# Performance work log

Hardware: AMD Instinct MI355X
Metric: run time of the kernel (lower is better)

Reference implementation:

```python
import jax, jax.numpy as jnp
import numpy as np

NUM_FEATURE = 512
HIDDEN = 256
NUM_CLASSES = 10
L1 = 1e-4
ALPHA = 1e-3
BATCH = 65536


def setup_inputs() -> dict:
    key = jax.random.key(0)
    k = jax.random.split(key, 6)
    x = jax.random.normal(k[0], (BATCH, NUM_FEATURE), dtype=jnp.float32)
    y = jax.random.randint(k[1], (BATCH,), 0, NUM_CLASSES, dtype=jnp.int32)
    fc0 = jax.random.normal(k[2], (NUM_FEATURE, 512), dtype=jnp.float32) / NUM_FEATURE
    fc1 = jax.random.normal(k[3], (NUM_FEATURE, 512), dtype=jnp.float32) / NUM_FEATURE
    w = jax.random.normal(k[4], (NUM_FEATURE, HIDDEN), dtype=jnp.float32) / NUM_FEATURE
    w1 = jax.random.normal(k[5], (HIDDEN, NUM_CLASSES), dtype=jnp.float32) / HIDDEN
    return {"x": x, "y": y, "fc0": fc0, "fc1": fc1, "w": w, "w1": w1}


def reference(x, y, fc0, fc1, w, w1):
    # sigmoid-gated MLP block with residual
    x1 = x @ fc0                                   # [B, 512]
    x2 = jax.nn.relu(x @ fc1)                      # [B, 512]
    x4 = x + (1.0 + jax.nn.sigmoid(x1)) * x2       # [B, 512] residual

    # head (Dropout(p=0.0) is identity)
    logits = jax.nn.relu(x4 @ w) @ w1              # [B, 10]
    pred = jnp.argmax(logits, axis=1)

    # cross-entropy (mean over batch)
    logp = jax.nn.log_softmax(logits, axis=-1)
    ce = -jnp.mean(jnp.take_along_axis(logp, y[:, None].astype(jnp.int32), axis=1))

    # L1 penalty on all weight matrices
    l1_pen = L1 * (jnp.abs(w1).sum() + jnp.abs(w).sum()
                   + jnp.abs(fc0).sum() + jnp.abs(fc1).sum())

    # per-class variance: sum_i ||mean_{y_i} - x4_i||^2, vectorized via segment sums
    counts = jax.ops.segment_sum(jnp.ones((x4.shape[0],), jnp.float32), y,
                                 num_segments=NUM_CLASSES)
    sums = jax.ops.segment_sum(x4, y, num_segments=NUM_CLASSES)   # [10, 512]
    means = sums / jnp.maximum(counts, 1.0)[:, None]
    var_loss = jnp.sum(jnp.square(means[y] - x4))

    loss = ce + l1_pen + ALPHA * var_loss
    acc = jnp.mean((pred.astype(jnp.int32) == y.astype(jnp.int32)).astype(jnp.float32))
    return (loss, acc)
```

## Files before the change

### kernel.cpp

```cpp
#include <hip/hip_runtime.h>
#include <stdint.h>

#define BATCH 65536
#define FDIM 512
#define HDIM 256
#define NC 10
#define NREP 16

typedef short short8 __attribute__((ext_vector_type(8)));
typedef float f32x4 __attribute__((ext_vector_type(4)));

#define OFF_FC0T   ((size_t)0)
#define OFF_FC1T   (OFF_FC0T + (size_t)512*512*2)
#define OFF_WT     (OFF_FC1T + (size_t)512*512*2)
#define OFF_XT     (OFF_WT   + (size_t)256*512*2)
#define OFF_X4T    (OFF_XT   + (size_t)BATCH*512*2)
#define OFF_ACC    (OFF_X4T  + (size_t)BATCH*512*2)
#define SCAL_SUMSQ 0
#define SCAL_CE    16
#define SCAL_ACC   32
#define SCAL_L1    48
#define SCAL_CTR   64
#define SCAL_N     128
#define CNT_OFF    SCAL_N
#define GSUM_OFF   (SCAL_N + NREP*16)
#define ACC_FLOATS (GSUM_OFF + NREP*5120)
#define OFF_W1T    (OFF_ACC + (size_t)ACC_FLOATS*4)

#define GLL(g,l) __builtin_amdgcn_global_load_lds((const __attribute__((address_space(1))) void*)(g), (__attribute__((address_space(3))) void*)(l), 16, 0, 0)

__device__ __forceinline__ unsigned short f2b(float f){
  unsigned u = __float_as_uint(f);
  u += 0x7FFFu + ((u >> 16) & 1u);
  return (unsigned short)(u >> 16);
}
__device__ __forceinline__ float b2f(unsigned short h){
  return __uint_as_float(((unsigned)h) << 16);
}
__device__ __forceinline__ unsigned pk2b(float f0, float f1){
  unsigned u0 = __float_as_uint(f0) + 0x8000u;
  unsigned u1 = __float_as_uint(f1) + 0x8000u;
  return __builtin_amdgcn_perm(u1, u0, 0x07060302u);
}
__device__ __forceinline__ float ald(const float* p){
  return __hip_atomic_load(p, __ATOMIC_RELAXED, __HIP_MEMORY_SCOPE_AGENT);
}

__global__ __launch_bounds__(256) void k_setup(
    const float* __restrict__ x,   const float* __restrict__ fc0,
    const float* __restrict__ fc1, const float* __restrict__ w,
    const float* __restrict__ w1,  const int* __restrict__ y,
    unsigned short* __restrict__ xT,   unsigned short* __restrict__ fc0T,
    unsigned short* __restrict__ fc1T, unsigned short* __restrict__ wT,
    unsigned short* __restrict__ w1T,  float* __restrict__ accb)
{
  int blk = blockIdx.x, t = threadIdx.x;
  if (blk < 2048){
    __shared__ __align__(16) unsigned short xls[16*520];
    int wv = t >> 6, l = t & 63;
    #pragma unroll 1
    for (int it = 0; it < 2; ++it){
      int I = blk*2 + it;
      #pragma unroll
      for (int rr = 0; rr < 4; ++rr){
        int row = wv*4 + rr;
        const float* src = x + ((size_t)(I*16 + row))*FDIM + l*8;
        float4 v0 = *(const float4*)src;
        float4 v1 = *(const float4*)(src + 4);
        unsigned o[4];
        o[0] = pk2b(v0.x, v0.y); o[1] = pk2b(v0.z, v0.w);
        o[2] = pk2b(v1.x, v1.y); o[3] = pk2b(v1.z, v1.w);
        *(short8*)&xls[row*520 + l*8] = *(short8*)o;
      }
      __syncthreads();
      #pragma unroll
      for (int cc = 0; cc < 4; ++cc){
        int C = cc*4 + wv;
        short8 v = *(const short8*)&xls[(l & 15)*520 + C*32 + (l >> 4)*8];
        *(short8*)&xT[(((size_t)I*16 + C) << 9) + l*8] = v;
      }
      __syncthreads();
    }
    return;
  }
  if (blk < 2384){
    int i = (blk - 2048)*256 + t;
    float l1v = 0.f;
    if (i < 32768){
      int n4 = i&15, m = (i>>4)&3, C = (i>>6)&15, J = i>>10;
      int n = J*16+n4, k8 = C*4+m;
      unsigned short o[8];
      #pragma unroll
      for (int j=0;j<8;++j){ float v = fc0[(size_t)(k8*8+j)*512 + n]; o[j]=f2b(v); l1v += fabsf(v); }
      *(short8*)&fc0T[(size_t)(J*16+C)*512 + (i&63)*8] = *(short8*)o;
    } else if (i < 65536){
      int j0 = i - 32768;
      int n4 = j0&15, m = (j0>>4)&3, C = (j0>>6)&15, J = j0>>10;
      int n = J*16+n4, k8 = C*4+m;
      unsigned short o[8];
      #pragma unroll
      for (int j=0;j<8;++j){ float v = fc1[(size_t)(k8*8+j)*512 + n]; o[j]=f2b(v); l1v += fabsf(v); }
      *(short8*)&fc1T[(size_t)(J*16+C)*512 + (j0&63)*8] = *(short8*)o;
    } else if (i < 81920){
      int j0 = i - 65536;
      int n4 = j0&15, m = (j0>>4)&3, C = (j0>>6)&15, J = j0>>10;
      int n = J*16+n4, k8 = C*4+m;
      unsigned short o[8];
      #pragma unroll
      for (int j=0;j<8;++j){ float v = w[(size_t)(k8*8+j)*256 + n]; o[j]=f2b(v); l1v += fabsf(v); }
      *(short8*)&wT[(size_t)(J*16+C)*512 + (j0&63)*8] = *(short8*)o;
    } else if (i < 86016){
      int j0 = i - 81920;
      int C = j0 >> 9, l = (j0 >> 3) & 63, e = j0 & 7;
      int n = l & 15, k = C*32 + (l>>4)*8 + e;
      float v = (n < NC) ? w1[k*NC + n] : 0.f;
      w1T[C*512 + l*8 + e] = f2b(v);
      if (n < NC) l1v = fabsf(v);
    }
    for (int off = 32; off; off >>= 1) l1v += __shfl_down(l1v, off);
    if ((t & 63) == 0 && l1v != 0.f)
      atomicAdd(&accb[SCAL_L1 + (blk & (NREP-1))], l1v);
    return;
  }
  if (blk < 2465){
    int base = (blk - 2384)*1024;
    #pragma unroll
    for (int j=0;j<4;++j){
      int idx = base + j*256 + t;
      if (idx < ACC_FLOATS && (idx < CNT_OFF || idx >= CNT_OFF + NREP*16))
        accb[idx] = 0.f;
    }
    return;
  }
  {
    __shared__ float cntS[16];
    int b = blk - 2465;
    if (t < 16) cntS[t] = 0.f;
    __syncthreads();
    int base = b*4096;
    for (int i = t; i < 4096; i += 256) atomicAdd(&cntS[y[base+i]], 1.f);
    __syncthreads();
    if (t < 16) accb[CNT_OFF + b*16 + t] = cntS[t];
  }
}

__global__ __launch_bounds__(512, 4) void k_gemm12(
    const unsigned short* __restrict__ xT,
    const unsigned short* __restrict__ fc0T,
    const unsigned short* __restrict__ fc1T,
    const int* __restrict__ y,
    unsigned short* __restrict__ x4T,
    float* __restrict__ accb)
{
  extern __shared__ __align__(16) char ldsd[];
  float* scal = accb;
  float* gsum = accb + GSUM_OFF;

  int blk = blockIdx.x;
  int wg = (blk & 7)*256 + (blk >> 3);
  int rowblk = wg >> 2;
  int colblk = wg & 3;

  int t = threadIdx.x;
  int wv = t >> 6, lane = t & 63, ln = lane & 15, quad = lane >> 4;
  int wr = wv >> 2, wc = wv & 3;

  const char* xb  = (const char*)xT;
  const char* b0b = (const char*)fc0T;
  const char* b1b = (const char*)fc1T;

  const f32x4 zv = {0.f,0.f,0.f,0.f};
  f32x4 acc1[4][2], acc2[4][2];
  #pragma unroll
  for (int m=0;m<4;++m){ acc1[m][0]=zv; acc1[m][1]=zv; acc2[m][0]=zv; acc2[m][1]=zv; }

  short8 a[4], b0r[2], b1r[2];

  GLL(xb  + (((size_t)((rowblk*8+wv)*16 + 0)) << 10) + lane*16, ldsd +         (wv<<10) + lane*16);
  GLL(b0b + (((size_t)((colblk*8+wv)*16 + 0)) << 10) + lane*16, ldsd +  8192 + (wv<<10) + lane*16);
  GLL(b1b + (((size_t)((colblk*8+wv)*16 + 0)) << 10) + lane*16, ldsd + 16384 + (wv<<10) + lane*16);
  asm volatile("s_waitcnt vmcnt(0)" ::: "memory");
  __builtin_amdgcn_sched_barrier(0);
  __builtin_amdgcn_s_barrier();

  #pragma unroll
  for (int kt = 0; kt < 16; ++kt){
    char* cur = ldsd + ((kt & 1) ? 24576 : 0);
    char* nxt = ldsd + ((kt & 1) ? 0 : 24576);
    if (kt < 15){
      GLL(xb  + (((size_t)((rowblk*8+wv)*16 + kt+1)) << 10) + lane*16, nxt +         (wv<<10) + lane*16);
      GLL(b0b + (((size_t)((colblk*8+wv)*16 + kt+1)) << 10) + lane*16, nxt +  8192 + (wv<<10) + lane*16);
      GLL(b1b + (((size_t)((colblk*8+wv)*16 + kt+1)) << 10) + lane*16, nxt + 16384 + (wv<<10) + lane*16);
    }
    #pragma unroll
    for (int m=0;m<4;++m)
      a[m] = *(const short8*)(cur + ((wr*4+m)<<10) + lane*16);
    #pragma unroll
    for (int n=0;n<2;++n){
      b0r[n] = *(const short8*)(cur +  8192 + ((wc*2+n)<<10) + lane*16);
      b1r[n] = *(const short8*)(cur + 16384 + ((wc*2+n)<<10) + lane*16);
    }
    asm volatile("s_waitcnt lgkmcnt(0)" ::: "memory");
    __builtin_amdgcn_sched_barrier(0);
    __builtin_amdgcn_s_setprio(1);
    #pragma unroll
    for (int n=0;n<2;++n)
      #pragma unroll
      for (int m=0;m<4;++m){
        acc1[m][n] = __builtin_amdgcn_mfma_f32_16x16x32_bf16(a[m], b0r[n], acc1[m][n], 0,0,0);
        acc2[m][n] = __builtin_amdgcn_mfma_f32_16x16x32_bf16(a[m], b1r[n], acc2[m][n], 0,0,0);
      }
    __builtin_amdgcn_s_setprio(0);
    if (kt < 15){ asm volatile("s_waitcnt vmcnt(0)" ::: "memory"); }
    __builtin_amdgcn_sched_barrier(0);
    __builtin_amdgcn_s_barrier();
  }

  #pragma unroll
  for (int c = 0; c < 4; ++c){
    GLL(xb + (((size_t)((rowblk*8+wv)*16 + colblk*4 + c)) << 10) + lane*16,
        ldsd + ((wv*4 + c) << 10) + lane*16);
  }
  asm volatile("s_waitcnt vmcnt(0)" ::: "memory");
  __syncthreads();

  unsigned short* resU = (unsigned short*)ldsd;
  unsigned short* x4U  = (unsigned short*)(ldsd + 32768);
  float sumsq = 0.f;
  #pragma unroll
  for (int m = 0; m < 4; ++m){
    #pragma unroll
    for (int n = 0; n < 2; ++n){
      #pragma unroll
      for (int r = 0; r < 4; ++r){
        int slot = (quad*4 + r) | ((n*2 + (ln>>3)) << 4);
        int idx = (((wr*4 + m)*4 + wc) << 9) + slot*8 + (ln & 7);
        float xv  = b2f(resU[idx]);
        float x1v = acc1[m][n][r];
        float x2v = fmaxf(acc2[m][n][r], 0.f);
        float gate = 1.f + 1.f/(1.f + __expf(-x1v));
        float x4v = fmaf(gate, x2v, xv);
        unsigned short ub = f2b(x4v);
        float fq = b2f(ub);
        sumsq = fmaf(fq, fq, sumsq);
        x4U[idx] = ub;
        acc1[m][n][r] = fq;
      }
    }
  }
  for (int off = 32; off; off >>= 1) sumsq += __shfl_down(sumsq, off);
  __syncthreads();

  float cs[NC][2];
  #pragma unroll
  for (int c=0;c<NC;++c){ cs[c][0]=0.f; cs[c][1]=0.f; }
  {
    const int* yrow = y + rowblk*128 + wr*64;
    #pragma unroll
    for (int m = 0; m < 4; ++m){
      int yv[4];
      #pragma unroll
      for (int r = 0; r < 4; ++r) yv[r] = yrow[m*16 + quad*4 + r];
      #pragma unroll
      for (int r = 0; r < 4; ++r){
        float v0 = acc1[m][0][r], v1 = acc1[m][1][r];
        #pragma unroll
        for (int c = 0; c < NC; ++c){
          bool msk = (yv[r] == c);
          cs[c][0] += msk ? v0 : 0.f;
          cs[c][1] += msk ? v1 : 0.f;
        }
      }
    }
  }
  #pragma unroll
  for (int c = 0; c < NC; ++c)
    #pragma unroll
    for (int n = 0; n < 2; ++n){
      cs[c][n] += __shfl_xor(cs[c][n], 16);
      cs[c][n] += __shfl_xor(cs[c][n], 32);
    }
  if (lane < 16){
    size_t gb = (size_t)(blk & (NREP-1))*5120 + colblk*128 + wc*32 + ln;
    #pragma unroll
    for (int c = 0; c < NC; ++c){
      atomicAdd(&gsum[gb + c*512],      cs[c][0]);
      atomicAdd(&gsum[gb + c*512 + 16], cs[c][1]);
    }
  }

  float* red = (float*)ldsd;
  if (lane == 0) red[wv] = sumsq;
  __syncthreads();
  if (t == 0){
    float s = 0.f;
    #pragma unroll
    for (int i=0;i<8;++i) s += red[i];
    atomicAdd(&scal[SCAL_SUMSQ + (blk & (NREP-1))], s);
  }
  #pragma unroll
  for (int r = 0; r < 4; ++r){
    int o = r*512 + t;
    int tile = o >> 6, off16 = o & 63;
    int Il = tile >> 2, Cl = tile & 3;
    size_t Ig = (size_t)rowblk*8 + Il;
    int Cg = colblk*4 + Cl;
    *(short8*)&x4T[((Ig*16 + Cg) << 9) + off16*8] =
      *(const short8*)&x4U[(tile << 9) + off16*8];
  }
}


#define BARRIER() __builtin_amdgcn_s_barrier()
#define LGKM0() do{ asm volatile("s_waitcnt lgkmcnt(0)" ::: "memory"); \
                    __builtin_amdgcn_sched_barrier(0); }while(0)

#define RA(AB, C) do{                                                         \
  _Pragma("unroll") for (int m_=0;m_<8;++m_)                                  \
    a[m_] = *(const short8*)((AB) + (((wr*8+m_)*2 + (C))<<10) + lane*16);     \
}while(0)

#define RB(AB, MAT, C) do{                                                    \
  _Pragma("unroll") for (int n_=0;n_<2;++n_)                                  \
    bb[n_] = *(const short8*)((AB) + 32768 + (MAT)*16384 +                    \
                              (((wc*2+n_)*2 + (C))<<10) + lane*16);           \
}while(0)

#define MM16(ACC) do{                                                         \
  __builtin_amdgcn_s_setprio(1);                                              \
  _Pragma("unroll") for (int n_=0;n_<2;++n_)                                  \
  _Pragma("unroll") for (int m_=0;m_<8;++m_)                                  \
    ACC[m_][n_] = __builtin_amdgcn_mfma_f32_16x16x32_bf16(a[m_], bb[n_], ACC[m_][n_], 0,0,0); \
  __builtin_amdgcn_s_setprio(0);                                              \
}while(0)

#define SA(KT, C) do{                                                         \
  char* d_ = ldsd + (((KT)&1) ? 65536 : 0);                                   \
  _Pragma("unroll") for (int r_=0;r_<2;++r_){                                 \
    int I_ = wv + r_*8;                                                       \
    GLL(xb + (((size_t)((rowblk*16 + I_)*16 + (KT)*2 + (C))) << 10) + lane*16,\
        d_ + ((I_*2 + (C)) << 10) + lane*16);                                 \
  } }while(0)

#define SB(KT, C) do{                                                         \
  char* d_ = ldsd + (((KT)&1) ? 65536 : 0) + 32768;                           \
  GLL(b0b + (((size_t)((colblk*8 + wv)*16 + (KT)*2 + (C))) << 10) + lane*16,  \
      d_ + ((wv*2 + (C)) << 10) + lane*16);                                   \
  GLL(b1b + (((size_t)((colblk*8 + wv)*16 + (KT)*2 + (C))) << 10) + lane*16,  \
      d_ + 16384 + ((wv*2 + (C)) << 10) + lane*16);                           \
}while(0)

#define KLOOP() do{                                                           \
  SA(0,0); SB(0,0); SA(0,1); SB(0,1); SA(1,0); SB(1,0); SA(1,1);              \
  asm volatile("s_waitcnt vmcnt(6)" ::: "memory");                            \
  __builtin_amdgcn_sched_barrier(0);                                          \
  BARRIER();                                                                  \
  _Pragma("unroll")                                                           \
  for (int i = 0; i < 4; ++i){                                                \
    int kt0 = 2*i, kt1 = 2*i+1;                                               \
    char* Ab0 = ldsd + ((kt0 & 1) ? 65536 : 0);                               \
    char* Ab1 = ldsd + ((kt1 & 1) ? 65536 : 0);                               \
    RA(Ab0, 0); RB(Ab0, 0, 0);                                                \
    SB(kt1, 1);                                                               \
    BARRIER(); LGKM0(); MM16(acc1);                                           \
    BARRIER();                                                                \
    RB(Ab0, 1, 0);                                                            \
    if (i < 3) SA(kt0+2, 0);                                                  \
    BARRIER(); LGKM0(); MM16(acc2);                                           \
    BARRIER();                                                                \
    RA(Ab0, 1); RB(Ab0, 0, 1);                                                \
    if (i < 3) SB(kt0+2, 0);                                                  \
    BARRIER(); LGKM0(); MM16(acc1);                                           \
    BARRIER();                                                                \
    RB(Ab0, 1, 1);                                                            \
    if (i < 3) SA(kt0+2, 1);                                                  \
    BARRIER(); LGKM0(); MM16(acc2);                                           \
    if (i < 3) { asm volatile("s_waitcnt vmcnt(6)" ::: "memory"); }           \
    else       { asm volatile("s_waitcnt vmcnt(0)" ::: "memory"); }           \
    __builtin_amdgcn_sched_barrier(0);                                        \
    BARRIER();                                                                \
    RA(Ab1, 0); RB(Ab1, 0, 0);                                                \
    if (i < 3) SB(kt0+2, 1);                                                  \
    BARRIER(); LGKM0(); MM16(acc1);                                           \
    BARRIER();                                                                \
    RB(Ab1, 1, 0);                                                            \
    if (i < 3) SA(kt1+2, 0);                                                  \
    BARRIER(); LGKM0(); MM16(acc2);                                           \
    BARRIER();                                                                \
    RA(Ab1, 1); RB(Ab1, 0, 1);                                                \
    if (i < 3) SB(kt1+2, 0);                                                  \
    BARRIER(); LGKM0(); MM16(acc1);                                           \
    BARRIER();                                                                \
    RB(Ab1, 1, 1);                                                            \
    if (i < 3) SA(kt1+2, 1);                                                  \
    BARRIER(); LGKM0(); MM16(acc2);                                           \
    if (i < 3) { asm volatile("s_waitcnt vmcnt(6)" ::: "memory");             \
                 __builtin_amdgcn_sched_barrier(0); }                         \
    BARRIER();                                                                \
  }                                                                           \
}while(0)

__global__ __launch_bounds__(512, 2) void k_gemm3_head(
    const unsigned short* __restrict__ x4T,
    const unsigned short* __restrict__ wT,
    const unsigned short* __restrict__ w1T,
    const int* __restrict__ y,
    float* __restrict__ accb,
    float* __restrict__ out)
{
  extern __shared__ __align__(16) char ldsd[];
  __shared__ float redc[8], reda[8];
  __shared__ int lastB;

  float* scal = accb;

  int blk = blockIdx.x;
  int rowblk = blk;
  const int colblk = 0;

  int t = threadIdx.x;
  int wv = t >> 6, lane = t & 63, ln = lane & 15, quad = lane >> 4;
  int wr = wv >> 2, wc = wv & 3;
  int rep = (blk ^ (blk >> 4)) & (NREP-1);

  const char* xb  = (const char*)x4T;
  const char* b0b = (const char*)wT;
  const char* b1b = (const char*)wT + (size_t)128*1024;

  const f32x4 zv = {0.f,0.f,0.f,0.f};
  f32x4 acc1[8][2], acc2[8][2];
  #pragma unroll
  for (int m=0;m<8;++m){ acc1[m][0]=zv; acc1[m][1]=zv; acc2[m][0]=zv; acc2[m][1]=zv; }

  short8 a[8], bb[2];

  KLOOP();

  short8 bw1[8];
  #pragma unroll
  for (int Ck = 0; Ck < 8; ++Ck)
    bw1[Ck] = *(const short8*)&w1T[Ck*512 + lane*8];

  unsigned short* transH = (unsigned short*)ldsd;
  #pragma unroll
  for (int m = 0; m < 8; ++m){
    #pragma unroll
    for (int n = 0; n < 2; ++n){
      #pragma unroll
      for (int r = 0; r < 4; ++r){
        int slot = (quad*4 + r) | ((n*2 + (ln>>3)) << 4);
        int e = ln & 7;
        int IhA = wr*8 + m;
        transH[((IhA*8 + wc)     << 9) + slot*8 + e] = f2b(fmaxf(acc1[m][n][r], 0.f));
        transH[((IhA*8 + 4 + wc) << 9) + slot*8 + e] = f2b(fmaxf(acc2[m][n][r], 0.f));
      }
    }
  }
  __syncthreads();

  f32x4 alog[2] = {zv, zv};
  #pragma unroll
  for (int ih = 0; ih < 2; ++ih){
    int Ih = wv*2 + ih;
    #pragma unroll
    for (int Ck = 0; Ck < 8; ++Ck){
      short8 af = *(const short8*)&transH[((Ih*8 + Ck) << 9) + lane*8];
      alog[ih] = __builtin_amdgcn_mfma_f32_16x16x32_bf16(af, bw1[Ck], alog[ih], 0,0,0);
    }
  }

  float ce_l = 0.f, acc_l = 0.f;
  #pragma unroll
  for (int ih = 0; ih < 2; ++ih){
    #pragma unroll
    for (int r = 0; r < 4; ++r){
      int grow = blk*256 + (wv*2 + ih)*16 + quad*4 + r;
      int yv = y[grow];
      float lg = (ln < NC) ? alog[ih][r] : -1e30f;
      float m = lg; int mi = ln;
      #pragma unroll
      for (int mk = 1; mk < 16; mk <<= 1){
        float om = __shfl_xor(m, mk); int oi = __shfl_xor(mi, mk);
        if (om > m || (om == m && oi < mi)){ m = om; mi = oi; }
      }
      float e  = (ln < NC) ? __expf(lg - m) : 0.f;
      float sy = (ln == yv) ? lg : 0.f;
      #pragma unroll
      for (int mk = 1; mk < 16; mk <<= 1){ e += __shfl_xor(e, mk); sy += __shfl_xor(sy, mk); }
      float lse = m + __logf(e);
      if (ln == 0){ ce_l += (lse - sy); acc_l += (mi == yv) ? 1.f : 0.f; }
    }
  }
  ce_l  += __shfl_down(ce_l, 16);  acc_l += __shfl_down(acc_l, 16);
  ce_l  += __shfl_down(ce_l, 32);  acc_l += __shfl_down(acc_l, 32);
  if (lane == 0){ redc[wv] = ce_l; reda[wv] = acc_l; }
  __syncthreads();
  if (t == 0){
    float c = 0.f, aa = 0.f;
    #pragma unroll
    for (int i=0;i<8;++i){ c += redc[i]; aa += reda[i]; }
    atomicAdd(&scal[SCAL_CE  + rep], c);
    atomicAdd(&scal[SCAL_ACC + rep], aa);
    __threadfence();
    int prev = atomicAdd((int*)(scal + SCAL_CTR), 1);
    lastB = (prev == (int)gridDim.x - 1);
  }
  __syncthreads();
  if (!lastB) return;

  {
    const float* gsum = accb + GSUM_OFF;
    const float* gcnt = accb + CNT_OFF;
    float contrib = 0.f;
    for (int idx = t; idx < 5120; idx += 512){
      float S = 0.f;
      #pragma unroll
      for (int r = 0; r < NREP; ++r) S += ald(&gsum[(size_t)r*5120 + idx]);
      int c = idx >> 9;
      float cnt = 0.f;
      #pragma unroll
      for (int r = 0; r < NREP; ++r) cnt += ald(&gcnt[r*16 + c]);
      contrib += S*S / fmaxf(cnt, 1.f);
    }
    for (int off = 32; off; off >>= 1) contrib += __shfl_down(contrib, off);
    __syncthreads();
    if (lane == 0) redc[wv] = contrib;
    __syncthreads();
    if (t == 0){
      float var2 = 0.f;
      #pragma unroll
      for (int i=0;i<8;++i) var2 += redc[i];
      float sumsq=0.f, ce=0.f, accv=0.f, l1=0.f;
      for (int r=0;r<NREP;++r){
        sumsq += ald(&scal[SCAL_SUMSQ+r]);
        ce    += ald(&scal[SCAL_CE+r]);
        accv  += ald(&scal[SCAL_ACC+r]);
        l1    += ald(&scal[SCAL_L1+r]);
      }
      float var_loss = sumsq - var2;
      out[0] = ce/(float)BATCH + 1e-4f*l1 + 1e-3f*var_loss;
      out[1] = accv/(float)BATCH;
    }
  }
}

extern "C" void kernel_launch(void* const* d_in, const int* in_sizes, int n_in,
                              void* d_out, int out_size, void* d_ws, size_t ws_size,
                              hipStream_t stream){
  (void)in_sizes; (void)n_in; (void)out_size; (void)ws_size;
  const float* x   = (const float*)d_in[0];
  const int*   y   = (const int*)d_in[1];
  const float* fc0 = (const float*)d_in[2];
  const float* fc1 = (const float*)d_in[3];
  const float* w   = (const float*)d_in[4];
  const float* w1  = (const float*)d_in[5];
  char* ws = (char*)d_ws;
  unsigned short* fc0T = (unsigned short*)(ws + OFF_FC0T);
  unsigned short* fc1T = (unsigned short*)(ws + OFF_FC1T);
  unsigned short* wT   = (unsigned short*)(ws + OFF_WT);
  unsigned short* xT   = (unsigned short*)(ws + OFF_XT);
  unsigned short* x4T  = (unsigned short*)(ws + OFF_X4T);
  unsigned short* w1T  = (unsigned short*)(ws + OFF_W1T);
  float* accb = (float*)(ws + OFF_ACC);

  static bool once = [](){
    hipFuncSetAttribute((const void*)k_gemm12,
                        hipFuncAttributeMaxDynamicSharedMemorySize, 65536);
    hipFuncSetAttribute((const void*)k_gemm3_head,
                        hipFuncAttributeMaxDynamicSharedMemorySize, 131072);
    return true;
  }();
  (void)once;

  k_setup<<<2481, 256, 0, stream>>>(x, fc0, fc1, w, w1, y, xT, fc0T, fc1T, wT, w1T, accb);
  k_gemm12<<<2048, 512, 65536, stream>>>(xT, fc0T, fc1T, y, x4T, accb);
  k_gemm3_head<<<256, 512, 131072, stream>>>(x4T, wT, w1T, y, accb, (float*)d_out);
}
```

Baseline: 352.2 us.

## Fuse x fp32-to-bf16 conversion into gemm12 A-tile loads, drop xT pre-pass

Removes the separate setup pass that converted x to a bf16 tiled copy (xT) and instead has k_gemm12 read fp32 x directly into registers, pack it to bf16 and write it into LDS each k-step. This drops one full write and read of a 64 MB bf16 copy of x plus the setup blocks for it. In exchange, each of the 4 column blocks re-reads the fp32 row tile (twice the bytes of bf16), the A loads are now register-staged rather than direct-to-LDS, and the residual reload also reads fp32.

```diff
diff --git a/kernel.cpp b/kernel.cpp
--- a/kernel.cpp
+++ b/kernel.cpp
@@ -13,8 +13,7 @@
 #define OFF_FC0T   ((size_t)0)
 #define OFF_FC1T   (OFF_FC0T + (size_t)512*512*2)
 #define OFF_WT     (OFF_FC1T + (size_t)512*512*2)
-#define OFF_XT     (OFF_WT   + (size_t)256*512*2)
-#define OFF_X4T    (OFF_XT   + (size_t)BATCH*512*2)
+#define OFF_X4T    (OFF_WT   + (size_t)256*512*2)
 #define OFF_ACC    (OFF_X4T  + (size_t)BATCH*512*2)
 #define SCAL_SUMSQ 0
 #define SCAL_CE    16
@@ -47,44 +46,16 @@
 }
 
 __global__ __launch_bounds__(256) void k_setup(
-    const float* __restrict__ x,   const float* __restrict__ fc0,
-    const float* __restrict__ fc1, const float* __restrict__ w,
-    const float* __restrict__ w1,  const int* __restrict__ y,
-    unsigned short* __restrict__ xT,   unsigned short* __restrict__ fc0T,
-    unsigned short* __restrict__ fc1T, unsigned short* __restrict__ wT,
-    unsigned short* __restrict__ w1T,  float* __restrict__ accb)
+    const float* __restrict__ fc0, const float* __restrict__ fc1,
+    const float* __restrict__ w,   const float* __restrict__ w1,
+    const int* __restrict__ y,
+    unsigned short* __restrict__ fc0T, unsigned short* __restrict__ fc1T,
+    unsigned short* __restrict__ wT,   unsigned short* __restrict__ w1T,
+    float* __restrict__ accb)
 {
   int blk = blockIdx.x, t = threadIdx.x;
-  if (blk < 2048){
-    __shared__ __align__(16) unsigned short xls[16*520];
-    int wv = t >> 6, l = t & 63;
-    #pragma unroll 1
-    for (int it = 0; it < 2; ++it){
-      int I = blk*2 + it;
-      #pragma unroll
-      for (int rr = 0; rr < 4; ++rr){
-        int row = wv*4 + rr;
-        const float* src = x + ((size_t)(I*16 + row))*FDIM + l*8;
-        float4 v0 = *(const float4*)src;
-        float4 v1 = *(const float4*)(src + 4);
-        unsigned o[4];
-        o[0] = pk2b(v0.x, v0.y); o[1] = pk2b(v0.z, v0.w);
-        o[2] = pk2b(v1.x, v1.y); o[3] = pk2b(v1.z, v1.w);
-        *(short8*)&xls[row*520 + l*8] = *(short8*)o;
-      }
-      __syncthreads();
-      #pragma unroll
-      for (int cc = 0; cc < 4; ++cc){
-        int C = cc*4 + wv;
-        short8 v = *(const short8*)&xls[(l & 15)*520 + C*32 + (l >> 4)*8];
-        *(short8*)&xT[(((size_t)I*16 + C) << 9) + l*8] = v;
-      }
-      __syncthreads();
-    }
-    return;
-  }
-  if (blk < 2384){
-    int i = (blk - 2048)*256 + t;
+  if (blk < 336){
+    int i = blk*256 + t;
     float l1v = 0.f;
     if (i < 32768){
       int n4 = i&15, m = (i>>4)&3, C = (i>>6)&15, J = i>>10;
@@ -122,8 +93,8 @@
       atomicAdd(&accb[SCAL_L1 + (blk & (NREP-1))], l1v);
     return;
   }
-  if (blk < 2465){
-    int base = (blk - 2384)*1024;
+  if (blk < 417){
+    int base = (blk - 336)*1024;
     #pragma unroll
     for (int j=0;j<4;++j){
       int idx = base + j*256 + t;
@@ -134,7 +105,7 @@
   }
   {
     __shared__ float cntS[16];
-    int b = blk - 2465;
+    int b = blk - 417;
     if (t < 16) cntS[t] = 0.f;
     __syncthreads();
     int base = b*4096;
@@ -145,7 +116,7 @@
 }
 
 __global__ __launch_bounds__(512, 4) void k_gemm12(
-    const unsigned short* __restrict__ xT,
+    const float* __restrict__ x,
     const unsigned short* __restrict__ fc0T,
     const unsigned short* __restrict__ fc1T,
     const int* __restrict__ y,
@@ -165,9 +136,9 @@
   int wv = t >> 6, lane = t & 63, ln = lane & 15, quad = lane >> 4;
   int wr = wv >> 2, wc = wv & 3;
 
-  const char* xb  = (const char*)xT;
   const char* b0b = (const char*)fc0T;
   const char* b1b = (const char*)fc1T;
+  const float* arow = x + (size_t)(rowblk*128 + wv*16 + ln)*FDIM + quad*8;
 
   const f32x4 zv = {0.f,0.f,0.f,0.f};
   f32x4 acc1[4][2], acc2[4][2];
@@ -176,19 +147,28 @@
 
   short8 a[4], b0r[2], b1r[2];
 
-  GLL(xb  + (((size_t)((rowblk*8+wv)*16 + 0)) << 10) + lane*16, ldsd +         (wv<<10) + lane*16);
-  GLL(b0b + (((size_t)((colblk*8+wv)*16 + 0)) << 10) + lane*16, ldsd +  8192 + (wv<<10) + lane*16);
-  GLL(b1b + (((size_t)((colblk*8+wv)*16 + 0)) << 10) + lane*16, ldsd + 16384 + (wv<<10) + lane*16);
-  asm volatile("s_waitcnt vmcnt(0)" ::: "memory");
-  __builtin_amdgcn_sched_barrier(0);
-  __builtin_amdgcn_s_barrier();
+  {
+    float4 va0 = *(const float4*)(arow);
+    float4 va1 = *(const float4*)(arow + 4);
+    GLL(b0b + (((size_t)((colblk*8+wv)*16 + 0)) << 10) + lane*16, ldsd +  8192 + (wv<<10) + lane*16);
+    GLL(b1b + (((size_t)((colblk*8+wv)*16 + 0)) << 10) + lane*16, ldsd + 16384 + (wv<<10) + lane*16);
+    unsigned o[4];
+    o[0] = pk2b(va0.x, va0.y); o[1] = pk2b(va0.z, va0.w);
+    o[2] = pk2b(va1.x, va1.y); o[3] = pk2b(va1.z, va1.w);
+    *(short8*)(ldsd + (wv<<10) + lane*16) = *(short8*)o;
+    asm volatile("s_waitcnt vmcnt(0) lgkmcnt(0)" ::: "memory");
+    __builtin_amdgcn_sched_barrier(0);
+    __builtin_amdgcn_s_barrier();
+  }
 
   #pragma unroll
   for (int kt = 0; kt < 16; ++kt){
     char* cur = ldsd + ((kt & 1) ? 24576 : 0);
     char* nxt = ldsd + ((kt & 1) ? 0 : 24576);
+    float4 va0, va1;
     if (kt < 15){
-      GLL(xb  + (((size_t)((rowblk*8+wv)*16 + kt+1)) << 10) + lane*16, nxt +         (wv<<10) + lane*16);
+      va0 = *(const float4*)(arow + (kt+1)*32);
+      va1 = *(const float4*)(arow + (kt+1)*32 + 4);
       GLL(b0b + (((size_t)((colblk*8+wv)*16 + kt+1)) << 10) + lane*16, nxt +  8192 + (wv<<10) + lane*16);
       GLL(b1b + (((size_t)((colblk*8+wv)*16 + kt+1)) << 10) + lane*16, nxt + 16384 + (wv<<10) + lane*16);
     }
@@ -211,17 +191,27 @@
         acc2[m][n] = __builtin_amdgcn_mfma_f32_16x16x32_bf16(a[m], b1r[n], acc2[m][n], 0,0,0);
       }
     __builtin_amdgcn_s_setprio(0);
-    if (kt < 15){ asm volatile("s_waitcnt vmcnt(0)" ::: "memory"); }
+    if (kt < 15){
+      unsigned o[4];
+      o[0] = pk2b(va0.x, va0.y); o[1] = pk2b(va0.z, va0.w);
+      o[2] = pk2b(va1.x, va1.y); o[3] = pk2b(va1.z, va1.w);
+      *(short8*)(nxt + (wv<<10) + lane*16) = *(short8*)o;
+      asm volatile("s_waitcnt vmcnt(0) lgkmcnt(0)" ::: "memory");
+    }
     __builtin_amdgcn_sched_barrier(0);
     __builtin_amdgcn_s_barrier();
   }
 
   #pragma unroll
   for (int c = 0; c < 4; ++c){
-    GLL(xb + (((size_t)((rowblk*8+wv)*16 + colblk*4 + c)) << 10) + lane*16,
-        ldsd + ((wv*4 + c) << 10) + lane*16);
-  }
-  asm volatile("s_waitcnt vmcnt(0)" ::: "memory");
+    const float* rsrc = arow + (colblk*4 + c)*32;
+    float4 v0 = *(const float4*)rsrc;
+    float4 v1 = *(const float4*)(rsrc + 4);
+    unsigned o[4];
+    o[0] = pk2b(v0.x, v0.y); o[1] = pk2b(v0.z, v0.w);
+    o[2] = pk2b(v1.x, v1.y); o[3] = pk2b(v1.z, v1.w);
+    *(short8*)(ldsd + ((wv*4 + c) << 10) + lane*16) = *(short8*)o;
+  }
   __syncthreads();
 
   unsigned short* resU = (unsigned short*)ldsd;
@@ -558,7 +548,6 @@
   unsigned short* fc0T = (unsigned short*)(ws + OFF_FC0T);
   unsigned short* fc1T = (unsigned short*)(ws + OFF_FC1T);
   unsigned short* wT   = (unsigned short*)(ws + OFF_WT);
-  unsigned short* xT   = (unsigned short*)(ws + OFF_XT);
   unsigned short* x4T  = (unsigned short*)(ws + OFF_X4T);
   unsigned short* w1T  = (unsigned short*)(ws + OFF_W1T);
   float* accb = (float*)(ws + OFF_ACC);
@@ -572,7 +561,7 @@
   }();
   (void)once;
 
-  k_setup<<<2481, 256, 0, stream>>>(x, fc0, fc1, w, w1, y, xT, fc0T, fc1T, wT, w1T, accb);
-  k_gemm12<<<2048, 512, 65536, stream>>>(xT, fc0T, fc1T, y, x4T, accb);
+  k_setup<<<433, 256, 0, stream>>>(fc0, fc1, w, w1, y, fc0T, fc1T, wT, w1T, accb);
+  k_gemm12<<<2048, 512, 65536, stream>>>(x, fc0T, fc1T, y, x4T, accb);
   k_gemm3_head<<<256, 512, 131072, stream>>>(x4T, wT, w1T, y, accb, (float*)d_out);
 }
```

Measured after the change: 388.1 us. +10.2%, slower.
